# Kernel tuning notes

Measured on AMD Instinct MI355X. Metric: run time of the kernel, lower is better.

Reference implementation:

```python
import jax, jax.numpy as jnp
import numpy as np

TAU = 1.0  # temperature for function-mixing softmax


def setup_inputs() -> dict:
    key = jax.random.key(0)
    k1, k2, k3, k4 = jax.random.split(key, 4)
    B, IN, OUT, K = 256, 1024, 1024, 3
    return {
        "h": jax.random.normal(k1, (B, IN), dtype=jnp.float32),
        "W": jax.random.normal(k2, (OUT, IN), dtype=jnp.float32) * 0.05,
        "b": jax.random.normal(k3, (OUT,), dtype=jnp.float32) * 0.01,
        "f_logits": jax.random.normal(k4, (OUT, IN, K), dtype=jnp.float32),
    }


def reference(h, W, b, f_logits):
    # Function-mixing probabilities over K atoms: (out, in, K)
    p = jax.nn.softmax(f_logits / TAU, axis=-1)
    # Atom-transformed weights, atoms = [identity, tanh, sin]
    Wk = jnp.stack([W, jnp.tanh(W), jnp.sin(W)], axis=-1)  # (out, in, K)
    W_eff = jnp.sum(p * Wk, axis=-1)  # (out, in)
    # Broadcast multiply: (B, 1, in) * (1, out, in) -> (B, out, in)
    z = h[:, None, :] * W_eff[None, :, :]
    gz = jnp.tanh(z)  # g_fn (is_last=False)
    return jnp.sum(gz, axis=-1) + b[None, :]  # (B, out)
```

## Files before the change

kernel.cpp:

```cpp
#include <hip/hip_runtime.h>

typedef __attribute__((ext_vector_type(8))) short short8;
typedef __attribute__((ext_vector_type(4))) float floatx4;

__device__ __forceinline__ float fast_exp2(float x) { return __builtin_amdgcn_exp2f(x); }
__device__ __forceinline__ float fast_rcp(float x)  { return __builtin_amdgcn_rcpf(x); }

__device__ __forceinline__ unsigned short f2bf(float f) {
    union { float f; unsigned u; } v; v.f = f;
    unsigned u = v.u;
    return (unsigned short)((u + 0x7FFFu + ((u >> 16) & 1u)) >> 16);
}

#define B_DIM   256
#define IN_DIM  1024
#define OUT_DIM 1024
#define NK      5
#define KFEAT   (NK * IN_DIM)
#define LOG2E   1.4426950408889634f

#define NSEG    8
#define SEGK    (KFEAT / NSEG)
#define WSEGK   (SEGK / 4)

#define TC0 (1.0f)
#define TC1 (-0.3333333333f)
#define TC2 (0.1333333333f)
#define TC3 (-0.05396825397f)
#define TC4 (0.02186948853f)

__global__ __launch_bounds__(256) void feat_fused_kernel(
    const float* __restrict__ h,
    const float* __restrict__ W,
    const float* __restrict__ fl,
    unsigned short* __restrict__ Af,
    unsigned short* __restrict__ Bf)
{
    if (blockIdx.x < 1024) {
        const int j4 = blockIdx.x * 256 + threadIdx.x;
        const int o  = j4 >> 8;
        const int i  = (j4 & 255) * 4;
        const float4* fl4 = (const float4*)fl;
        float4 f0 = fl4[3 * j4 + 0];
        float4 f1 = fl4[3 * j4 + 1];
        float4 f2 = fl4[3 * j4 + 2];
        float4 w4 = ((const float4*)W)[j4];

        float l[4][3] = {{f0.x, f0.y, f0.z},
                         {f0.w, f1.x, f1.y},
                         {f1.z, f1.w, f2.x},
                         {f2.y, f2.z, f2.w}};
        float wv[4] = {w4.x, w4.y, w4.z, w4.w};
        const float C[NK] = {TC0, TC1, TC2, TC3, TC4};

        float we[4], tt[4];
#pragma unroll
        for (int e = 0; e < 4; ++e) {
            float e0 = fast_exp2(l[e][0] * LOG2E);
            float e1 = fast_exp2(l[e][1] * LOG2E);
            float e2 = fast_exp2(l[e][2] * LOG2E);
            float inv = fast_rcp(e0 + e1 + e2);
            float w = wv[e];
            float t = w * w;
            float th = w * (1.0f + t * (-0.3333333333f + t * (0.1333333333f + t * (-0.05396825397f))));
            float sn = w * (1.0f + t * (-0.1666666667f + t * (0.008333333333f + t * (-1.984126984e-4f))));
            we[e] = (e0 * w + e1 * th + e2 * sn) * inv;
            tt[e] = we[e] * we[e];
        }
#pragma unroll
        for (int s = 0; s < NK; ++s) {
            ushort4 u = make_ushort4(f2bf(C[s] * we[0]), f2bf(C[s] * we[1]),
                                     f2bf(C[s] * we[2]), f2bf(C[s] * we[3]));
            *(ushort4*)(Bf + (size_t)o * KFEAT + s * IN_DIM + i) = u;
#pragma unroll
            for (int e = 0; e < 4; ++e) we[e] *= tt[e];
        }
    } else {
        const int j4 = (blockIdx.x - 1024) * 256 + threadIdx.x;
        const int b  = j4 >> 8;
        const int i  = (j4 & 255) * 4;
        float4 hv = ((const float4*)h)[j4];
        float x[4] = {hv.x, hv.y, hv.z, hv.w};
        float p[4], t[4];
#pragma unroll
        for (int e = 0; e < 4; ++e) { p[e] = x[e]; t[e] = x[e] * x[e]; }
#pragma unroll
        for (int s = 0; s < NK; ++s) {
            ushort4 u = make_ushort4(f2bf(p[0]), f2bf(p[1]), f2bf(p[2]), f2bf(p[3]));
            *(ushort4*)(Af + (size_t)b * KFEAT + s * IN_DIM + i) = u;
#pragma unroll
            for (int e = 0; e < 4; ++e) p[e] *= t[e];
        }
    }
}

__global__ __launch_bounds__(256, 2) void gemm_feat_kernel(
    const unsigned short* __restrict__ Af,
    const unsigned short* __restrict__ Bf,
    float* __restrict__ part)
{
    __shared__ float red[4][64 * 64];

    const int bx = blockIdx.x;
    const int sg = bx & 7;
    const int tm = (bx >> 3) & 3;
    const int tn = bx >> 5;
    const int w    = threadIdx.x >> 6;
    const int lane = threadIdx.x & 63;
    const int q    = lane >> 4;
    const int ln   = lane & 15;

    const int kstart = sg * SEGK + w * WSEGK + q * 8;

    const short8* Ar[4];
    const short8* Br[4];
#pragma unroll
    for (int g = 0; g < 4; ++g)
        Ar[g] = (const short8*)(Af + (size_t)(tm * 64 + g * 16 + ln) * KFEAT + kstart);
#pragma unroll
    for (int c = 0; c < 4; ++c)
        Br[c] = (const short8*)(Bf + (size_t)(tn * 64 + c * 16 + ln) * KFEAT + kstart);

    floatx4 acc[4][4];
#pragma unroll
    for (int g = 0; g < 4; ++g)
#pragma unroll
        for (int c = 0; c < 4; ++c) acc[g][c] = (floatx4)(0.0f);

#pragma unroll
    for (int kk = 0; kk < WSEGK; kk += 32) {
        short8 a[4], b[4];
#pragma unroll
        for (int g = 0; g < 4; ++g) a[g] = Ar[g][kk >> 3];
#pragma unroll
        for (int c = 0; c < 4; ++c) b[c] = Br[c][kk >> 3];
#pragma unroll
        for (int g = 0; g < 4; ++g)
#pragma unroll
            for (int c = 0; c < 4; ++c)
                acc[g][c] = __builtin_amdgcn_mfma_f32_16x16x32_bf16(a[g], b[c], acc[g][c], 0, 0, 0);
    }

    float* my = &red[w][0];
#pragma unroll
    for (int g = 0; g < 4; ++g)
#pragma unroll
        for (int c = 0; c < 4; ++c)
#pragma unroll
            for (int r = 0; r < 4; ++r)
                my[(g * 16 + q * 4 + r) * 64 + (c * 16 + ln)] = acc[g][c][r];
    __syncthreads();

    float* pseg = part + (size_t)sg * (B_DIM * OUT_DIM);
    const int t = threadIdx.x;
#pragma unroll
    for (int j = 0; j < 16; ++j) {
        const int idx = j * 256 + t;
        const float v = red[0][idx] + red[1][idx] + red[2][idx] + red[3][idx];
        const int lr = idx >> 6, lc = idx & 63;
        pseg[(size_t)(tm * 64 + lr) * OUT_DIM + tn * 64 + lc] = v;
    }
}

__global__ __launch_bounds__(256) void reduce_bias_kernel(
    const float* __restrict__ part,
    const float* __restrict__ bias,
    float* __restrict__ out)
{
    const int j4 = blockIdx.x * 256 + threadIdx.x;
    float4 a = ((const float4*)bias)[j4 & 255];
#pragma unroll
    for (int s = 0; s < NSEG; ++s) {
        float4 p = ((const float4*)part)[s * 65536 + j4];
        a.x += p.x; a.y += p.y; a.z += p.z; a.w += p.w;
    }
    ((float4*)out)[j4] = a;
}

extern "C" void kernel_launch(void* const* d_in, const int* in_sizes, int n_in,
                              void* d_out, int out_size, void* d_ws, size_t ws_size,
                              hipStream_t stream) {
    const float* h  = (const float*)d_in[0];
    const float* W  = (const float*)d_in[1];
    const float* b  = (const float*)d_in[2];
    const float* fl = (const float*)d_in[3];
    float* out = (float*)d_out;

    unsigned short* Af = (unsigned short*)d_ws;
    unsigned short* Bf = Af + (size_t)B_DIM * KFEAT;
    float* part = (float*)(Bf + (size_t)OUT_DIM * KFEAT);

    feat_fused_kernel<<<1280, 256, 0, stream>>>(h, W, fl, Af, Bf);
    gemm_feat_kernel<<<512, 256, 0, stream>>>(Af, Bf, part);
    reduce_bias_kernel<<<256, 256, 0, stream>>>(part, b, out);
}
```

Baseline: 87.41 us.

## Fuse three kernels into one cooperative kernel with grid syncs

Replaces the three launches (feature build, split-K GEMM, reduce plus bias) with a single cooperative kernel of 512 blocks that uses grid.sync between phases. Each block builds two rows of Bf and some blocks also build Af rows. The LDS reduction buffer shrinks from four warp tiles to two by having warps 2-3 accumulate into the slots of warps 0-1. The aim is to remove launch gaps, at the cost of grid-wide barrier overhead and lower per-phase parallelism. The old three-kernel path stays as a fallback if the cooperative launch fails.

Result: slower. 281.8 us (+222.4%).

```diff
diff --git a/kernel.cpp b/kernel.cpp
--- a/kernel.cpp
+++ b/kernel.cpp
@@ -1,4 +1,7 @@
 #include <hip/hip_runtime.h>
+#include <hip/hip_cooperative_groups.h>
+
+namespace cg = cooperative_groups;
 
 typedef __attribute__((ext_vector_type(8))) short short8;
 typedef __attribute__((ext_vector_type(4))) float floatx4;
@@ -29,69 +32,196 @@
 #define TC3 (-0.05396825397f)
 #define TC4 (0.02186948853f)
 
+
+__device__ __forceinline__ void bf_unit(int o, int tid,
+                                        const float* __restrict__ W,
+                                        const float* __restrict__ fl,
+                                        unsigned short* __restrict__ Bf)
+{
+    const int j4 = o * 256 + tid;
+    const int i  = (j4 & 255) * 4;
+    const float4* fl4 = (const float4*)fl;
+    float4 f0 = fl4[3 * j4 + 0];
+    float4 f1 = fl4[3 * j4 + 1];
+    float4 f2 = fl4[3 * j4 + 2];
+    float4 w4 = ((const float4*)W)[j4];
+
+    float l[4][3] = {{f0.x, f0.y, f0.z},
+                     {f0.w, f1.x, f1.y},
+                     {f1.z, f1.w, f2.x},
+                     {f2.y, f2.z, f2.w}};
+    float wv[4] = {w4.x, w4.y, w4.z, w4.w};
+    const float C[NK] = {TC0, TC1, TC2, TC3, TC4};
+
+    float we[4], tt[4];
+#pragma unroll
+    for (int e = 0; e < 4; ++e) {
+        float e0 = fast_exp2(l[e][0] * LOG2E);
+        float e1 = fast_exp2(l[e][1] * LOG2E);
+        float e2 = fast_exp2(l[e][2] * LOG2E);
+        float inv = fast_rcp(e0 + e1 + e2);
+        float w = wv[e];
+        float t = w * w;
+        float th = w * (1.0f + t * (-0.3333333333f + t * (0.1333333333f + t * (-0.05396825397f))));
+        float sn = w * (1.0f + t * (-0.1666666667f + t * (0.008333333333f + t * (-1.984126984e-4f))));
+        we[e] = (e0 * w + e1 * th + e2 * sn) * inv;
+        tt[e] = we[e] * we[e];
+    }
+#pragma unroll
+    for (int s = 0; s < NK; ++s) {
+        ushort4 u = make_ushort4(f2bf(C[s] * we[0]), f2bf(C[s] * we[1]),
+                                 f2bf(C[s] * we[2]), f2bf(C[s] * we[3]));
+        *(ushort4*)(Bf + (size_t)o * KFEAT + s * IN_DIM + i) = u;
+#pragma unroll
+        for (int e = 0; e < 4; ++e) we[e] *= tt[e];
+    }
+}
+
+__device__ __forceinline__ void af_unit(int b, int tid,
+                                        const float* __restrict__ h,
+                                        unsigned short* __restrict__ Af)
+{
+    const int j4 = b * 256 + tid;
+    const int i  = (j4 & 255) * 4;
+    float4 hv = ((const float4*)h)[j4];
+    float x[4] = {hv.x, hv.y, hv.z, hv.w};
+    float p[4], t[4];
+#pragma unroll
+    for (int e = 0; e < 4; ++e) { p[e] = x[e]; t[e] = x[e] * x[e]; }
+#pragma unroll
+    for (int s = 0; s < NK; ++s) {
+        ushort4 u = make_ushort4(f2bf(p[0]), f2bf(p[1]), f2bf(p[2]), f2bf(p[3]));
+        *(ushort4*)(Af + (size_t)b * KFEAT + s * IN_DIM + i) = u;
+#pragma unroll
+        for (int e = 0; e < 4; ++e) p[e] *= t[e];
+    }
+}
+
+__device__ __forceinline__ void gemm_body(int bx, int tid,
+                                          const unsigned short* __restrict__ Af,
+                                          const unsigned short* __restrict__ Bf,
+                                          float* __restrict__ part,
+                                          float* red )
+{
+    const int sg = bx & 7;
+    const int tm = (bx >> 3) & 3;
+    const int tn = bx >> 5;
+    const int w    = tid >> 6;
+    const int lane = tid & 63;
+    const int q    = lane >> 4;
+    const int ln   = lane & 15;
+
+    const int kstart = sg * SEGK + w * WSEGK + q * 8;
+
+    const short8* Ar[4];
+    const short8* Br[4];
+#pragma unroll
+    for (int g = 0; g < 4; ++g)
+        Ar[g] = (const short8*)(Af + (size_t)(tm * 64 + g * 16 + ln) * KFEAT + kstart);
+#pragma unroll
+    for (int c = 0; c < 4; ++c)
+        Br[c] = (const short8*)(Bf + (size_t)(tn * 64 + c * 16 + ln) * KFEAT + kstart);
+
+    floatx4 acc[4][4];
+#pragma unroll
+    for (int g = 0; g < 4; ++g)
+#pragma unroll
+        for (int c = 0; c < 4; ++c) acc[g][c] = (floatx4)(0.0f);
+
+#pragma unroll
+    for (int kk = 0; kk < WSEGK; kk += 32) {
+        short8 a[4], b[4];
+#pragma unroll
+        for (int g = 0; g < 4; ++g) a[g] = Ar[g][kk >> 3];
+#pragma unroll
+        for (int c = 0; c < 4; ++c) b[c] = Br[c][kk >> 3];
+#pragma unroll
+        for (int g = 0; g < 4; ++g)
+#pragma unroll
+            for (int c = 0; c < 4; ++c)
+                acc[g][c] = __builtin_amdgcn_mfma_f32_16x16x32_bf16(a[g], b[c], acc[g][c], 0, 0, 0);
+    }
+
+    float* buf = red + (size_t)(w & 1) * 4096;
+    if (w < 2) {
+#pragma unroll
+        for (int g = 0; g < 4; ++g)
+#pragma unroll
+            for (int c = 0; c < 4; ++c)
+#pragma unroll
+                for (int r = 0; r < 4; ++r)
+                    buf[(g * 16 + q * 4 + r) * 64 + (c * 16 + ln)] = acc[g][c][r];
+    }
+    __syncthreads();
+    if (w >= 2) {
+#pragma unroll
+        for (int g = 0; g < 4; ++g)
+#pragma unroll
+            for (int c = 0; c < 4; ++c)
+#pragma unroll
+                for (int r = 0; r < 4; ++r)
+                    buf[(g * 16 + q * 4 + r) * 64 + (c * 16 + ln)] += acc[g][c][r];
+    }
+    __syncthreads();
+
+    float* pseg = part + (size_t)sg * (B_DIM * OUT_DIM);
+#pragma unroll
+    for (int j = 0; j < 16; ++j) {
+        const int idx = j * 256 + tid;
+        const float v = red[idx] + red[4096 + idx];
+        const int lr = idx >> 6, lc = idx & 63;
+        pseg[(size_t)(tm * 64 + lr) * OUT_DIM + tn * 64 + lc] = v;
+    }
+}
+
+__device__ __forceinline__ void reduce_body(int bx, int tid,
+                                            const float* __restrict__ part,
+                                            const float* __restrict__ bias,
+                                            float* __restrict__ out)
+{
+    const int j4 = bx * 256 + tid;
+    float4 a = ((const float4*)bias)[j4 & 255];
+#pragma unroll
+    for (int s = 0; s < NSEG; ++s) {
+        float4 p = ((const float4*)part)[s * 65536 + j4];
+        a.x += p.x; a.y += p.y; a.z += p.z; a.w += p.w;
+    }
+    ((float4*)out)[j4] = a;
+}
+
+__global__ __launch_bounds__(256, 2) void fused_all(
+    const float* __restrict__ h, const float* __restrict__ W,
+    const float* __restrict__ fl, const float* __restrict__ bias,
+    unsigned short* __restrict__ Af, unsigned short* __restrict__ Bf,
+    float* __restrict__ part, float* __restrict__ out)
+{
+    __shared__ float red[2 * 4096];
+    const int bx  = blockIdx.x;
+    const int tid = threadIdx.x;
+    cg::grid_group grid = cg::this_grid();
+
+    bf_unit(bx, tid, W, fl, Bf);
+    bf_unit(bx + 512, tid, W, fl, Bf);
+    if (bx < 256) af_unit(bx, tid, h, Af);
+
+    __threadfence();
+    grid.sync();
+
+    gemm_body(bx, tid, Af, Bf, part, red);
+
+    __threadfence();
+    grid.sync();
+
+    if (bx < 256) reduce_body(bx, tid, part, bias, out);
+}
+
 __global__ __launch_bounds__(256) void feat_fused_kernel(
-    const float* __restrict__ h,
-    const float* __restrict__ W,
+    const float* __restrict__ h, const float* __restrict__ W,
     const float* __restrict__ fl,
-    unsigned short* __restrict__ Af,
-    unsigned short* __restrict__ Bf)
-{
-    if (blockIdx.x < 1024) {
-        const int j4 = blockIdx.x * 256 + threadIdx.x;
-        const int o  = j4 >> 8;
-        const int i  = (j4 & 255) * 4;
-        const float4* fl4 = (const float4*)fl;
-        float4 f0 = fl4[3 * j4 + 0];
-        float4 f1 = fl4[3 * j4 + 1];
-        float4 f2 = fl4[3 * j4 + 2];
-        float4 w4 = ((const float4*)W)[j4];
-
-        float l[4][3] = {{f0.x, f0.y, f0.z},
-                         {f0.w, f1.x, f1.y},
-                         {f1.z, f1.w, f2.x},
-                         {f2.y, f2.z, f2.w}};
-        float wv[4] = {w4.x, w4.y, w4.z, w4.w};
-        const float C[NK] = {TC0, TC1, TC2, TC3, TC4};
-
-        float we[4], tt[4];
-#pragma unroll
-        for (int e = 0; e < 4; ++e) {
-            float e0 = fast_exp2(l[e][0] * LOG2E);
-            float e1 = fast_exp2(l[e][1] * LOG2E);
-            float e2 = fast_exp2(l[e][2] * LOG2E);
-            float inv = fast_rcp(e0 + e1 + e2);
-            float w = wv[e];
-            float t = w * w;
-            float th = w * (1.0f + t * (-0.3333333333f + t * (0.1333333333f + t * (-0.05396825397f))));
-            float sn = w * (1.0f + t * (-0.1666666667f + t * (0.008333333333f + t * (-1.984126984e-4f))));
-            we[e] = (e0 * w + e1 * th + e2 * sn) * inv;
-            tt[e] = we[e] * we[e];
-        }
-#pragma unroll
-        for (int s = 0; s < NK; ++s) {
-            ushort4 u = make_ushort4(f2bf(C[s] * we[0]), f2bf(C[s] * we[1]),
-                                     f2bf(C[s] * we[2]), f2bf(C[s] * we[3]));
-            *(ushort4*)(Bf + (size_t)o * KFEAT + s * IN_DIM + i) = u;
-#pragma unroll
-            for (int e = 0; e < 4; ++e) we[e] *= tt[e];
-        }
-    } else {
-        const int j4 = (blockIdx.x - 1024) * 256 + threadIdx.x;
-        const int b  = j4 >> 8;
-        const int i  = (j4 & 255) * 4;
-        float4 hv = ((const float4*)h)[j4];
-        float x[4] = {hv.x, hv.y, hv.z, hv.w};
-        float p[4], t[4];
-#pragma unroll
-        for (int e = 0; e < 4; ++e) { p[e] = x[e]; t[e] = x[e] * x[e]; }
-#pragma unroll
-        for (int s = 0; s < NK; ++s) {
-            ushort4 u = make_ushort4(f2bf(p[0]), f2bf(p[1]), f2bf(p[2]), f2bf(p[3]));
-            *(ushort4*)(Af + (size_t)b * KFEAT + s * IN_DIM + i) = u;
-#pragma unroll
-            for (int e = 0; e < 4; ++e) p[e] *= t[e];
-        }
-    }
+    unsigned short* __restrict__ Af, unsigned short* __restrict__ Bf)
+{
+    if (blockIdx.x < 1024) bf_unit(blockIdx.x, threadIdx.x, W, fl, Bf);
+    else                   af_unit(blockIdx.x - 1024, threadIdx.x, h, Af);
 }
 
 __global__ __launch_bounds__(256, 2) void gemm_feat_kernel(
@@ -99,82 +229,15 @@
     const unsigned short* __restrict__ Bf,
     float* __restrict__ part)
 {
-    __shared__ float red[4][64 * 64];
-
-    const int bx = blockIdx.x;
-    const int sg = bx & 7;
-    const int tm = (bx >> 3) & 3;
-    const int tn = bx >> 5;
-    const int w    = threadIdx.x >> 6;
-    const int lane = threadIdx.x & 63;
-    const int q    = lane >> 4;
-    const int ln   = lane & 15;
-
-    const int kstart = sg * SEGK + w * WSEGK + q * 8;
-
-    const short8* Ar[4];
-    const short8* Br[4];
-#pragma unroll
-    for (int g = 0; g < 4; ++g)
-        Ar[g] = (const short8*)(Af + (size_t)(tm * 64 + g * 16 + ln) * KFEAT + kstart);
-#pragma unroll
-    for (int c = 0; c < 4; ++c)
-        Br[c] = (const short8*)(Bf + (size_t)(tn * 64 + c * 16 + ln) * KFEAT + kstart);
-
-    floatx4 acc[4][4];
-#pragma unroll
-    for (int g = 0; g < 4; ++g)
-#pragma unroll
-        for (int c = 0; c < 4; ++c) acc[g][c] = (floatx4)(0.0f);
-
-#pragma unroll
-    for (int kk = 0; kk < WSEGK; kk += 32) {
-        short8 a[4], b[4];
-#pragma unroll
-        for (int g = 0; g < 4; ++g) a[g] = Ar[g][kk >> 3];
-#pragma unroll
-        for (int c = 0; c < 4; ++c) b[c] = Br[c][kk >> 3];
-#pragma unroll
-        for (int g = 0; g < 4; ++g)
-#pragma unroll
-            for (int c = 0; c < 4; ++c)
-                acc[g][c] = __builtin_amdgcn_mfma_f32_16x16x32_bf16(a[g], b[c], acc[g][c], 0, 0, 0);
-    }
-
-    float* my = &red[w][0];
-#pragma unroll
-    for (int g = 0; g < 4; ++g)
-#pragma unroll
-        for (int c = 0; c < 4; ++c)
-#pragma unroll
-            for (int r = 0; r < 4; ++r)
-                my[(g * 16 + q * 4 + r) * 64 + (c * 16 + ln)] = acc[g][c][r];
-    __syncthreads();
-
-    float* pseg = part + (size_t)sg * (B_DIM * OUT_DIM);
-    const int t = threadIdx.x;
-#pragma unroll
-    for (int j = 0; j < 16; ++j) {
-        const int idx = j * 256 + t;
-        const float v = red[0][idx] + red[1][idx] + red[2][idx] + red[3][idx];
-        const int lr = idx >> 6, lc = idx & 63;
-        pseg[(size_t)(tm * 64 + lr) * OUT_DIM + tn * 64 + lc] = v;
-    }
+    __shared__ float red[2 * 4096];
+    gemm_body(blockIdx.x, threadIdx.x, Af, Bf, part, red);
 }
 
 __global__ __launch_bounds__(256) void reduce_bias_kernel(
-    const float* __restrict__ part,
-    const float* __restrict__ bias,
+    const float* __restrict__ part, const float* __restrict__ bias,
     float* __restrict__ out)
 {
-    const int j4 = blockIdx.x * 256 + threadIdx.x;
-    float4 a = ((const float4*)bias)[j4 & 255];
-#pragma unroll
-    for (int s = 0; s < NSEG; ++s) {
-        float4 p = ((const float4*)part)[s * 65536 + j4];
-        a.x += p.x; a.y += p.y; a.z += p.z; a.w += p.w;
-    }
-    ((float4*)out)[j4] = a;
+    reduce_body(blockIdx.x, threadIdx.x, part, bias, out);
 }
 
 extern "C" void kernel_launch(void* const* d_in, const int* in_sizes, int n_in,
@@ -190,7 +253,14 @@
     unsigned short* Bf = Af + (size_t)B_DIM * KFEAT;
     float* part = (float*)(Bf + (size_t)OUT_DIM * KFEAT);
 
-    feat_fused_kernel<<<1280, 256, 0, stream>>>(h, W, fl, Af, Bf);
-    gemm_feat_kernel<<<512, 256, 0, stream>>>(Af, Bf, part);
-    reduce_bias_kernel<<<256, 256, 0, stream>>>(part, b, out);
-}
+    void* args[] = {(void*)&h, (void*)&W, (void*)&fl, (void*)&b,
+                    (void*)&Af, (void*)&Bf, (void*)&part, (void*)&out};
+    hipError_t e = hipLaunchCooperativeKernel((const void*)fused_all,
+                                              dim3(512), dim3(256),
+                                              args, 0, stream);
+    if (e != hipSuccess) {
+        feat_fused_kernel<<<1280, 256, 0, stream>>>(h, W, fl, Af, Bf);
+        gemm_feat_kernel<<<512, 256, 0, stream>>>(Af, Bf, part);
+        reduce_bias_kernel<<<256, 256, 0, stream>>>(part, b, out);
+    }
+}
```
